# Kernel optimization log

Measured on AMD Instinct MI355X. Metric: run time of the kernel, lower is better.

Reference implementation:

```python
import jax, jax.numpy as jnp
import numpy as np

NUM_LAYERS = 2      # args.num_layers
EPS = 1e-6          # poincare_to_lorentz eps
NORM_CLIP = 1.0     # exp_map norm_control clip
N, K, F, D = 30000, 32, 256, 128


def _normalize_lorentz(h):
    # project onto hyperboloid: time = sqrt(1 + |space|^2)
    sp = h[:, 1:]
    t = jnp.sqrt(1.0 + jnp.sum(sp * sp, axis=-1, keepdims=True))
    return jnp.concatenate([t, sp], axis=-1)


def _exp_map_zero(v):
    # tangent vector at origin has zero time component (normalize_tan with x=0)
    sp = v[:, 1:]
    ldv = jnp.sum(sp * sp, axis=-1, keepdims=True)          # Lorentz norm^2 of (0, sp)
    nd = jnp.sqrt(jnp.clip(ldv + 1e-9, 1e-10, None))
    t = jnp.minimum(nd, NORM_CLIP)                           # norm_control
    time = jnp.cosh(t)
    space = jnp.sinh(t) * sp / nd
    return _normalize_lorentz(jnp.concatenate([time, space], axis=-1))


def _hyperbolic_mean(nbr, w):
    # nbr: [N, K, D] Lorentz points; w: [N, K] neighbor weights
    k = nbr[..., 1:] / nbr[..., :1]                          # h2k: Klein model
    kn = jnp.clip(jnp.sum(k * k, axis=-1, keepdims=True), 0.0, 0.9)
    lam = w[..., None] / jnp.sqrt(1.0 - kn)                  # weighted Lorentz factors
    k_mean = jnp.sum(lam * k, axis=1) / jnp.sum(lam, axis=1)  # [N, D-1]
    # k2h: Klein -> hyperboloid
    kn2 = jnp.minimum(jnp.sum(k_mean * k_mean, axis=-1, keepdims=True), 0.9)
    ones = jnp.ones((k_mean.shape[0], 1), k_mean.dtype)
    return jnp.concatenate([ones, k_mean], axis=-1) / jnp.sqrt(1.0 - kn2)


def _lorentz_activation(h):
    # lorentz -> poincare, SELU, poincare -> lorentz (c = 1)
    p = h[:, 1:] / (h[:, :1] + 1.0)
    p = jax.nn.selu(p)
    pn = jnp.sum(p * p, axis=-1, keepdims=True)
    return jnp.concatenate([1.0 + pn, 2.0 * p], axis=-1) / (1.0 - pn + EPS)


def setup_inputs() -> dict:
    key = jax.random.key(0)
    k1, k2, k3, k4, k5 = jax.random.split(key, 5)
    x = jax.random.normal(k1, (N, F), dtype=jnp.float32)
    adj = jax.random.randint(k2, (N, K), 0, N, dtype=jnp.int32)
    w = jax.random.uniform(k3, (N, K), dtype=jnp.float32)
    lin_W = jax.random.normal(k4, (F, D), dtype=jnp.float32) / np.sqrt(F)
    lin_b = jnp.zeros((D,), dtype=jnp.float32)
    M, _ = jnp.linalg.qr(jax.random.normal(k5, (D - 1, D - 1), dtype=jnp.float32))  # orthogonal init
    return {"x": x, "adj": adj, "w": w, "lin_W": lin_W, "lin_b": lin_b, "M": M}


def reference(x, adj, w, lin_W, lin_b, M):
    h = jax.nn.selu(x @ lin_W + lin_b)          # Euclidean projection + activation
    h = _exp_map_zero(h)                        # lift to hyperboloid
    d = h.shape[-1]
    # retrieve_params: block-diag [[1,0],[0,M]] Lorentz rotation (tie_weight -> shared)
    lw = jnp.zeros((d, d), h.dtype).at[0, 0].set(1.0).at[1:, 1:].set(M)
    for _ in range(NUM_LAYERS):
        msg = h @ lw                             # Stiefel transform
        nbr = msg[adj]                           # [N, K, D] neighbor gather
        h = _hyperbolic_mean(nbr, w)             # Klein weighted mean
        h = _lorentz_activation(h)               # SELU in Poincare model
        h = _normalize_lorentz(h)                # re-project onto hyperboloid
    return h
```

## Files before the change

### kernel.cpp

```cpp
#include <hip/hip_runtime.h>
#include <hip/hip_fp16.h>
#include <math.h>

#define NN 30000
#define KK 32
#define FF 256
#define DD 128
#define NB16 1875

typedef _Float16 f16x8 __attribute__((ext_vector_type(8)));
typedef float f32x4v __attribute__((ext_vector_type(4)));

__device__ __forceinline__ float seluf(float x) {
    const float scale = 1.0507009873554804934193349852946f;
    const float alpha = 1.6732632423543772848170429916717f;
    return x > 0.f ? scale * x : scale * alpha * expm1f(x);
}

__device__ __forceinline__ float waveReduceSum(float v) {
#pragma unroll
    for (int m = 1; m < 64; m <<= 1) v += __shfl_xor(v, m, 64);
    return v;
}

__global__ __launch_bounds__(256) void k_prep(
    const float* __restrict__ W, const float* __restrict__ M,
    _Float16* __restrict__ Wt, _Float16* __restrict__ Lt)
{
    const int b = blockIdx.x, t = threadIdx.x;
    if (b < 128) {
        Wt[b * FF + t] = (_Float16)W[t * DD + b];
    } else if (t < 128) {
        const int c = b - 128, k = t;
        const float v = (k == 0 && c == 0) ? 1.f
                      : ((k >= 1 && c >= 1) ? M[(k - 1) * 127 + (c - 1)] : 0.f);
        Lt[c * DD + k] = (_Float16)v;
    }
}

__global__ __launch_bounds__(256) void k_lin_exp_msg(
    const float* __restrict__ x, const _Float16* __restrict__ Wt,
    const float* __restrict__ b, const _Float16* __restrict__ Lt,
    __half* __restrict__ table)
{
    __shared__ float hs[16][132];
    __shared__ float red[4][16];
    __shared__ float m0s[16];
    const int wv_ = threadIdx.x >> 6;
    const int lane = threadIdx.x & 63;
    const int g = lane >> 4, c16 = lane & 15;
    const int baseRow = blockIdx.x * 16;
    const int nb = wv_ * 2;
    const int arow = baseRow + c16;

    f16x8 ahi[8];
    const float4* xp = (const float4*)(x + (size_t)arow * FF) + g * 2;
#pragma unroll
    for (int c = 0; c < 2; ++c) {
        float4 f[8];
#pragma unroll
        for (int kk = 0; kk < 4; ++kk) {
            f[2 * kk]     = xp[(c * 4 + kk) * 8];
            f[2 * kk + 1] = xp[(c * 4 + kk) * 8 + 1];
        }
#pragma unroll
        for (int kk = 0; kk < 4; ++kk) {
            const int ks = c * 4 + kk;
            const float q[8] = {f[2 * kk].x, f[2 * kk].y, f[2 * kk].z, f[2 * kk].w,
                                f[2 * kk + 1].x, f[2 * kk + 1].y, f[2 * kk + 1].z, f[2 * kk + 1].w};
#pragma unroll
            for (int j = 0; j < 8; ++j) ahi[ks][j] = (_Float16)q[j];
        }
    }

    f32x4v acc[2];
    acc[0] = acc[1] = f32x4v{0.f, 0.f, 0.f, 0.f};
#pragma unroll
    for (int ks = 0; ks < 8; ++ks) {
#pragma unroll
        for (int n = 0; n < 2; ++n) {
            const f16x8 bh = *(const f16x8*)(Wt + (size_t)((nb + n) * 16 + c16) * FF + ks * 32 + g * 8);
            acc[n] = __builtin_amdgcn_mfma_f32_16x16x32_f16(ahi[ks], bh, acc[n], 0, 0, 0);
        }
    }

    float bias[2];
#pragma unroll
    for (int n = 0; n < 2; ++n) bias[n] = b[(nb + n) * 16 + c16];

    float vv[4][2];
#pragma unroll
    for (int r = 0; r < 4; ++r) {
        float part = 0.f;
#pragma unroll
        for (int n = 0; n < 2; ++n) {
            vv[r][n] = seluf(acc[n][r] + bias[n]);
            float sq = vv[r][n] * vv[r][n];
            if (wv_ == 0 && n == 0 && c16 == 0) sq = 0.f;
            part += sq;
        }
#pragma unroll
        for (int m = 1; m < 16; m <<= 1) part += __shfl_xor(part, m, 64);
        if (c16 == 0) red[wv_][4 * g + r] = part;
    }
    __syncthreads();
#pragma unroll
    for (int r = 0; r < 4; ++r) {
        const int lrow = 4 * g + r;
        const float ldv = red[0][lrow] + red[1][lrow] + red[2][lrow] + red[3][lrow];
        const float nd = sqrtf(fmaxf(ldv + 1e-9f, 1e-10f));
        const float t  = fminf(nd, 1.0f);
        const float sc = sinhf(t) / nd;
        const float tm = sqrtf(1.f + sc * sc * ldv);
#pragma unroll
        for (int n = 0; n < 2; ++n) {
            const float o = (wv_ == 0 && n == 0 && c16 == 0) ? tm : sc * vv[r][n];
            hs[lrow][(nb + n) * 16 + c16] = o;
        }
    }
    __syncthreads();

    f16x8 mhi[4], mlo[4];
#pragma unroll
    for (int ks = 0; ks < 4; ++ks) {
        const float* hp = &hs[c16][ks * 32 + g * 8];
        const float4 f0 = *(const float4*)hp;
        const float4 f1 = *(const float4*)(hp + 4);
        const float q[8] = {f0.x, f0.y, f0.z, f0.w, f1.x, f1.y, f1.z, f1.w};
#pragma unroll
        for (int j = 0; j < 8; ++j) {
            mhi[ks][j] = (_Float16)q[j];
            mlo[ks][j] = (_Float16)(q[j] - (float)mhi[ks][j]);
        }
    }

    acc[0] = acc[1] = f32x4v{0.f, 0.f, 0.f, 0.f};
#pragma unroll
    for (int ks = 0; ks < 4; ++ks) {
#pragma unroll
        for (int n = 0; n < 2; ++n) {
            const f16x8 bh = *(const f16x8*)(Lt + (size_t)((nb + n) * 16 + c16) * DD + ks * 32 + g * 8);
            acc[n] = __builtin_amdgcn_mfma_f32_16x16x32_f16(mhi[ks], bh, acc[n], 0, 0, 0);
            acc[n] = __builtin_amdgcn_mfma_f32_16x16x32_f16(mlo[ks], bh, acc[n], 0, 0, 0);
        }
    }

#pragma unroll
    for (int r = 0; r < 4; ++r) {
        float part = 0.f;
#pragma unroll
        for (int n = 0; n < 2; ++n) {
            float sq = acc[n][r] * acc[n][r];
            if (wv_ == 0 && n == 0 && c16 == 0) sq = 0.f;
            part += sq;
        }
#pragma unroll
        for (int m = 1; m < 16; m <<= 1) part += __shfl_xor(part, m, 64);
        if (c16 == 0) red[wv_][4 * g + r] = part;
        if (wv_ == 0 && c16 == 0) m0s[4 * g + r] = acc[0][r];
    }
    __syncthreads();
#pragma unroll
    for (int r = 0; r < 4; ++r) {
        const int lrow = 4 * g + r;
        const int row = baseRow + lrow;
        const float rn = 1.f / m0s[lrow];
        const float sum2 = red[0][lrow] + red[1][lrow] + red[2][lrow] + red[3][lrow];
        float kn = sum2 * rn * rn;
        kn = fminf(fmaxf(kn, 0.f), 0.9f);
        const float fh = 1.f / sqrtf(1.f - kn);
#pragma unroll
        for (int n = 0; n < 2; ++n) {
            const float val = (wv_ == 0 && n == 0 && c16 == 0) ? fh : acc[n][r] * rn;
            table[(size_t)row * DD + (nb + n) * 16 + c16] = __float2half(val);
        }
    }
}

__global__ __launch_bounds__(256) void k_msg_aux(
    const float* __restrict__ h, const _Float16* __restrict__ Lt,
    __half* __restrict__ table)
{
    __shared__ float red[4][16];
    __shared__ float m0s[16];
    const int wv_ = threadIdx.x >> 6;
    const int lane = threadIdx.x & 63;
    const int g = lane >> 4, c16 = lane & 15;
    const int baseRow = blockIdx.x * 16;
    const int nb = wv_ * 2;
    const int arow = baseRow + c16;

    float4 f[8];
    const float4* hp = (const float4*)(h + (size_t)arow * DD) + g * 2;
#pragma unroll
    for (int ks = 0; ks < 4; ++ks) {
        f[2 * ks]     = hp[ks * 8];
        f[2 * ks + 1] = hp[ks * 8 + 1];
    }
    f16x8 ahi[4], alo[4];
#pragma unroll
    for (int ks = 0; ks < 4; ++ks) {
        const float q[8] = {f[2 * ks].x, f[2 * ks].y, f[2 * ks].z, f[2 * ks].w,
                            f[2 * ks + 1].x, f[2 * ks + 1].y, f[2 * ks + 1].z, f[2 * ks + 1].w};
#pragma unroll
        for (int j = 0; j < 8; ++j) {
            ahi[ks][j] = (_Float16)q[j];
            alo[ks][j] = (_Float16)(q[j] - (float)ahi[ks][j]);
        }
    }

    f32x4v acc[2];
    acc[0] = acc[1] = f32x4v{0.f, 0.f, 0.f, 0.f};
#pragma unroll
    for (int ks = 0; ks < 4; ++ks) {
#pragma unroll
        for (int n = 0; n < 2; ++n) {
            const f16x8 bh = *(const f16x8*)(Lt + (size_t)((nb + n) * 16 + c16) * DD + ks * 32 + g * 8);
            acc[n] = __builtin_amdgcn_mfma_f32_16x16x32_f16(ahi[ks], bh, acc[n], 0, 0, 0);
            acc[n] = __builtin_amdgcn_mfma_f32_16x16x32_f16(alo[ks], bh, acc[n], 0, 0, 0);
        }
    }

#pragma unroll
    for (int r = 0; r < 4; ++r) {
        float part = 0.f;
#pragma unroll
        for (int n = 0; n < 2; ++n) {
            float sq = acc[n][r] * acc[n][r];
            if (wv_ == 0 && n == 0 && c16 == 0) sq = 0.f;
            part += sq;
        }
#pragma unroll
        for (int m = 1; m < 16; m <<= 1) part += __shfl_xor(part, m, 64);
        if (c16 == 0) red[wv_][4 * g + r] = part;
        if (wv_ == 0 && c16 == 0) m0s[4 * g + r] = acc[0][r];
    }
    __syncthreads();
#pragma unroll
    for (int r = 0; r < 4; ++r) {
        const int lrow = 4 * g + r;
        const int row = baseRow + lrow;
        const float rn = 1.f / m0s[lrow];
        const float sum2 = red[0][lrow] + red[1][lrow] + red[2][lrow] + red[3][lrow];
        float kn = sum2 * rn * rn;
        kn = fminf(fmaxf(kn, 0.f), 0.9f);
        const float fh = 1.f / sqrtf(1.f - kn);
#pragma unroll
        for (int n = 0; n < 2; ++n) {
            const float val = (wv_ == 0 && n == 0 && c16 == 0) ? fh : acc[n][r] * rn;
            table[(size_t)row * DD + (nb + n) * 16 + c16] = __float2half(val);
        }
    }
}

__global__ __launch_bounds__(256) void k_layer(
    const __half* __restrict__ table, const int* __restrict__ adj,
    const float* __restrict__ w, float* __restrict__ out)
{
    const int wave = threadIdx.x >> 6;
    const int lane = threadIdx.x & 63;
    const int node = blockIdx.x * 4 + wave;

    const int   av = adj[node * KK + (lane & 31)];
    const float wv = w[node * KK + (lane & 31)];

    unsigned int vbits[32];
#pragma unroll
    for (int j = 0; j < KK; ++j) {
        const int idx = __shfl(av, j, 64);
        vbits[j] = *(const unsigned int*)(table + (size_t)idx * DD + lane * 2);
    }

    const float f  = __half2float(table[(size_t)av * DD]);
    const float lam = wv * f;
    float ls = lam;
#pragma unroll
    for (int m = 1; m < 32; m <<= 1) ls += __shfl_xor(ls, m, 64);

    float km0 = 0.f, km1 = 0.f;
#pragma unroll
    for (int j = 0; j < KK; ++j) {
        const float cj = __shfl(lam, j, 64);
        const __half2 hh = *(const __half2*)&vbits[j];
        const float2 v = __half22float2(hh);
        km0 = fmaf(cj, v.x, km0);
        km1 = fmaf(cj, v.y, km1);
    }
    const float rl = 1.f / ls;
    const float m0 = km0 * rl;
    const float m1 = km1 * rl;
    float c2 = (lane ? m0 * m0 : 0.f) + m1 * m1;
    const float kn2 = fminf(waveReduceSum(c2), 0.9f);
    const float invs = 1.f / sqrtf(1.f - kn2);
    const float pd = invs + 1.f;
    const float p0 = lane ? seluf(m0 * invs / pd) : 0.f;
    const float p1 = seluf(m1 * invs / pd);
    float pc = p0 * p0 + p1 * p1;
    const float pn = waveReduceSum(pc);
    const float rdn = 1.f / (1.f - pn + 1e-6f);
    const float tm = sqrtf(1.f + 4.f * pn * rdn * rdn);
    float2 o;
    o.x = lane ? 2.f * p0 * rdn : tm;
    o.y = 2.f * p1 * rdn;
    *(float2*)(out + (size_t)node * DD + lane * 2) = o;
}

extern "C" void kernel_launch(void* const* d_in, const int* in_sizes, int n_in,
                              void* d_out, int out_size, void* d_ws, size_t ws_size,
                              hipStream_t stream) {
    const float* x     = (const float*)d_in[0];
    const int*   adj   = (const int*)d_in[1];
    const float* w     = (const float*)d_in[2];
    const float* lin_W = (const float*)d_in[3];
    const float* lin_b = (const float*)d_in[4];
    const float* M     = (const float*)d_in[5];
    float*  h     = (float*)d_out;
    char*   ws    = (char*)d_ws;
    __half*   table = (__half*)ws;
    _Float16* Wt    = (_Float16*)(ws + 7680000);
    _Float16* Lt    = (_Float16*)(ws + 7745536);

    k_prep<<<256, 256, 0, stream>>>(lin_W, M, Wt, Lt);
    k_lin_exp_msg<<<NB16, 256, 0, stream>>>(x, Wt, lin_b, Lt, table);
    k_layer<<<NN / 4, 256, 0, stream>>>(table, adj, w, h);
    k_msg_aux<<<NB16, 256, 0, stream>>>(h, Lt, table);
    k_layer<<<NN / 4, 256, 0, stream>>>(table, adj, w, h);
}
```

Before: 132.7 us.

## Stage A operands in LDS once per block and preload B fragments

In both message kernels, each wave now loads only its slice of the input rows, converts it to fp16 (hi/lo split where used) and writes it to shared memory. All four waves then read the full A fragments from LDS, where before every wave redundantly loaded and converted the whole 16-row tile from global memory. The B fragments (Wt/Lt) are also hoisted into registers before the MFMA loops so loads can be issued ahead of the matrix ops. This costs an extra barrier, more LDS and higher register pressure.

```diff
diff --git a/kernel.cpp b/kernel.cpp
--- a/kernel.cpp
+++ b/kernel.cpp
@@ -7,6 +7,7 @@
 #define FF 256
 #define DD 128
 #define NB16 1875
+#define SA 268
 
 typedef _Float16 f16x8 __attribute__((ext_vector_type(8)));
 typedef float f32x4v __attribute__((ext_vector_type(4)));
@@ -43,7 +44,9 @@
     const float* __restrict__ b, const _Float16* __restrict__ Lt,
     __half* __restrict__ table)
 {
-    __shared__ float hs[16][132];
+    __shared__ _Float16 as_[16][SA];
+    __shared__ _Float16 hhi[16][SA];
+    __shared__ _Float16 hlo[16][SA];
     __shared__ float red[4][16];
     __shared__ float m0s[16];
     const int wv_ = threadIdx.x >> 6;
@@ -53,35 +56,39 @@
     const int nb = wv_ * 2;
     const int arow = baseRow + c16;
 
-    f16x8 ahi[8];
-    const float4* xp = (const float4*)(x + (size_t)arow * FF) + g * 2;
-#pragma unroll
-    for (int c = 0; c < 2; ++c) {
-        float4 f[8];
-#pragma unroll
-        for (int kk = 0; kk < 4; ++kk) {
-            f[2 * kk]     = xp[(c * 4 + kk) * 8];
-            f[2 * kk + 1] = xp[(c * 4 + kk) * 8 + 1];
-        }
-#pragma unroll
-        for (int kk = 0; kk < 4; ++kk) {
-            const int ks = c * 4 + kk;
-            const float q[8] = {f[2 * kk].x, f[2 * kk].y, f[2 * kk].z, f[2 * kk].w,
-                                f[2 * kk + 1].x, f[2 * kk + 1].y, f[2 * kk + 1].z, f[2 * kk + 1].w};
-#pragma unroll
-            for (int j = 0; j < 8; ++j) ahi[ks][j] = (_Float16)q[j];
-        }
-    }
+    {
+        const float4* xp = (const float4*)(x + (size_t)arow * FF);
+#pragma unroll
+        for (int i = 0; i < 2; ++i) {
+            const int ks = wv_ * 2 + i;
+            const float4 f0 = xp[ks * 8 + g * 2];
+            const float4 f1 = xp[ks * 8 + g * 2 + 1];
+            const float q[8] = {f0.x, f0.y, f0.z, f0.w, f1.x, f1.y, f1.z, f1.w};
+            f16x8 a;
+#pragma unroll
+            for (int j = 0; j < 8; ++j) a[j] = (_Float16)q[j];
+            *(f16x8*)&as_[c16][ks * 32 + g * 8] = a;
+        }
+    }
+    __syncthreads();
+
+    f16x8 bw0[8], bw1[8];
+#pragma unroll
+    for (int ks = 0; ks < 8; ++ks) {
+        bw0[ks] = *(const f16x8*)(Wt + (size_t)((nb + 0) * 16 + c16) * FF + ks * 32 + g * 8);
+        bw1[ks] = *(const f16x8*)(Wt + (size_t)((nb + 1) * 16 + c16) * FF + ks * 32 + g * 8);
+    }
+    f16x8 af[8];
+#pragma unroll
+    for (int ks = 0; ks < 8; ++ks)
+        af[ks] = *(const f16x8*)&as_[c16][ks * 32 + g * 8];
 
     f32x4v acc[2];
     acc[0] = acc[1] = f32x4v{0.f, 0.f, 0.f, 0.f};
 #pragma unroll
     for (int ks = 0; ks < 8; ++ks) {
-#pragma unroll
-        for (int n = 0; n < 2; ++n) {
-            const f16x8 bh = *(const f16x8*)(Wt + (size_t)((nb + n) * 16 + c16) * FF + ks * 32 + g * 8);
-            acc[n] = __builtin_amdgcn_mfma_f32_16x16x32_f16(ahi[ks], bh, acc[n], 0, 0, 0);
-        }
+        acc[0] = __builtin_amdgcn_mfma_f32_16x16x32_f16(af[ks], bw0[ks], acc[0], 0, 0, 0);
+        acc[1] = __builtin_amdgcn_mfma_f32_16x16x32_f16(af[ks], bw1[ks], acc[1], 0, 0, 0);
     }
 
     float bias[2];
@@ -114,35 +121,34 @@
         const float tm = sqrtf(1.f + sc * sc * ldv);
 #pragma unroll
         for (int n = 0; n < 2; ++n) {
+            const int col = (nb + n) * 16 + c16;
             const float o = (wv_ == 0 && n == 0 && c16 == 0) ? tm : sc * vv[r][n];
-            hs[lrow][(nb + n) * 16 + c16] = o;
-        }
-    }
-    __syncthreads();
-
-    f16x8 mhi[4], mlo[4];
-#pragma unroll
-    for (int ks = 0; ks < 4; ++ks) {
-        const float* hp = &hs[c16][ks * 32 + g * 8];
-        const float4 f0 = *(const float4*)hp;
-        const float4 f1 = *(const float4*)(hp + 4);
-        const float q[8] = {f0.x, f0.y, f0.z, f0.w, f1.x, f1.y, f1.z, f1.w};
-#pragma unroll
-        for (int j = 0; j < 8; ++j) {
-            mhi[ks][j] = (_Float16)q[j];
-            mlo[ks][j] = (_Float16)(q[j] - (float)mhi[ks][j]);
-        }
-    }
-
+            const _Float16 hi = (_Float16)o;
+            hhi[lrow][col] = hi;
+            hlo[lrow][col] = (_Float16)(o - (float)hi);
+        }
+    }
+    __syncthreads();
+
+    f16x8 bl0[4], bl1[4];
+#pragma unroll
+    for (int ks = 0; ks < 4; ++ks) {
+        bl0[ks] = *(const f16x8*)(Lt + (size_t)((nb + 0) * 16 + c16) * DD + ks * 32 + g * 8);
+        bl1[ks] = *(const f16x8*)(Lt + (size_t)((nb + 1) * 16 + c16) * DD + ks * 32 + g * 8);
+    }
+    f16x8 mh[4], ml[4];
+#pragma unroll
+    for (int ks = 0; ks < 4; ++ks) {
+        mh[ks] = *(const f16x8*)&hhi[c16][ks * 32 + g * 8];
+        ml[ks] = *(const f16x8*)&hlo[c16][ks * 32 + g * 8];
+    }
     acc[0] = acc[1] = f32x4v{0.f, 0.f, 0.f, 0.f};
 #pragma unroll
     for (int ks = 0; ks < 4; ++ks) {
-#pragma unroll
-        for (int n = 0; n < 2; ++n) {
-            const f16x8 bh = *(const f16x8*)(Lt + (size_t)((nb + n) * 16 + c16) * DD + ks * 32 + g * 8);
-            acc[n] = __builtin_amdgcn_mfma_f32_16x16x32_f16(mhi[ks], bh, acc[n], 0, 0, 0);
-            acc[n] = __builtin_amdgcn_mfma_f32_16x16x32_f16(mlo[ks], bh, acc[n], 0, 0, 0);
-        }
+        acc[0] = __builtin_amdgcn_mfma_f32_16x16x32_f16(mh[ks], bl0[ks], acc[0], 0, 0, 0);
+        acc[0] = __builtin_amdgcn_mfma_f32_16x16x32_f16(ml[ks], bl0[ks], acc[0], 0, 0, 0);
+        acc[1] = __builtin_amdgcn_mfma_f32_16x16x32_f16(mh[ks], bl1[ks], acc[1], 0, 0, 0);
+        acc[1] = __builtin_amdgcn_mfma_f32_16x16x32_f16(ml[ks], bl1[ks], acc[1], 0, 0, 0);
     }
 
 #pragma unroll
@@ -181,6 +187,8 @@
     const float* __restrict__ h, const _Float16* __restrict__ Lt,
     __half* __restrict__ table)
 {
+    __shared__ _Float16 hhi[16][SA];
+    __shared__ _Float16 hlo[16][SA];
     __shared__ float red[4][16];
     __shared__ float m0s[16];
     const int wv_ = threadIdx.x >> 6;
@@ -190,35 +198,43 @@
     const int nb = wv_ * 2;
     const int arow = baseRow + c16;
 
-    float4 f[8];
-    const float4* hp = (const float4*)(h + (size_t)arow * DD) + g * 2;
-#pragma unroll
-    for (int ks = 0; ks < 4; ++ks) {
-        f[2 * ks]     = hp[ks * 8];
-        f[2 * ks + 1] = hp[ks * 8 + 1];
-    }
-    f16x8 ahi[4], alo[4];
-#pragma unroll
-    for (int ks = 0; ks < 4; ++ks) {
-        const float q[8] = {f[2 * ks].x, f[2 * ks].y, f[2 * ks].z, f[2 * ks].w,
-                            f[2 * ks + 1].x, f[2 * ks + 1].y, f[2 * ks + 1].z, f[2 * ks + 1].w};
+    {
+        const float4* hp = (const float4*)(h + (size_t)arow * DD);
+        const int ks = wv_;
+        const float4 f0 = hp[ks * 8 + g * 2];
+        const float4 f1 = hp[ks * 8 + g * 2 + 1];
+        const float q[8] = {f0.x, f0.y, f0.z, f0.w, f1.x, f1.y, f1.z, f1.w};
+        f16x8 hi, lo;
 #pragma unroll
         for (int j = 0; j < 8; ++j) {
-            ahi[ks][j] = (_Float16)q[j];
-            alo[ks][j] = (_Float16)(q[j] - (float)ahi[ks][j]);
-        }
-    }
-
+            hi[j] = (_Float16)q[j];
+            lo[j] = (_Float16)(q[j] - (float)hi[j]);
+        }
+        *(f16x8*)&hhi[c16][ks * 32 + g * 8] = hi;
+        *(f16x8*)&hlo[c16][ks * 32 + g * 8] = lo;
+    }
+    __syncthreads();
+
+    f16x8 bl0[4], bl1[4];
+#pragma unroll
+    for (int ks = 0; ks < 4; ++ks) {
+        bl0[ks] = *(const f16x8*)(Lt + (size_t)((nb + 0) * 16 + c16) * DD + ks * 32 + g * 8);
+        bl1[ks] = *(const f16x8*)(Lt + (size_t)((nb + 1) * 16 + c16) * DD + ks * 32 + g * 8);
+    }
+    f16x8 mh[4], ml[4];
+#pragma unroll
+    for (int ks = 0; ks < 4; ++ks) {
+        mh[ks] = *(const f16x8*)&hhi[c16][ks * 32 + g * 8];
+        ml[ks] = *(const f16x8*)&hlo[c16][ks * 32 + g * 8];
+    }
     f32x4v acc[2];
     acc[0] = acc[1] = f32x4v{0.f, 0.f, 0.f, 0.f};
 #pragma unroll
     for (int ks = 0; ks < 4; ++ks) {
-#pragma unroll
-        for (int n = 0; n < 2; ++n) {
-            const f16x8 bh = *(const f16x8*)(Lt + (size_t)((nb + n) * 16 + c16) * DD + ks * 32 + g * 8);
-            acc[n] = __builtin_amdgcn_mfma_f32_16x16x32_f16(ahi[ks], bh, acc[n], 0, 0, 0);
-            acc[n] = __builtin_amdgcn_mfma_f32_16x16x32_f16(alo[ks], bh, acc[n], 0, 0, 0);
-        }
+        acc[0] = __builtin_amdgcn_mfma_f32_16x16x32_f16(mh[ks], bl0[ks], acc[0], 0, 0, 0);
+        acc[0] = __builtin_amdgcn_mfma_f32_16x16x32_f16(ml[ks], bl0[ks], acc[0], 0, 0, 0);
+        acc[1] = __builtin_amdgcn_mfma_f32_16x16x32_f16(mh[ks], bl1[ks], acc[1], 0, 0, 0);
+        acc[1] = __builtin_amdgcn_mfma_f32_16x16x32_f16(ml[ks], bl1[ks], acc[1], 0, 0, 0);
     }
 
 #pragma unroll
```

Result: faster. 119.5 us (-10.0%).
